# Performance work log

Measured on AMD Instinct MI355X. Metric: run time of the kernel, lower is better.

The kernel has to match this reference:

```python
import jax, jax.numpy as jnp
import numpy as np

D = 128
BITS = 3
N_LEVELS = 1 << BITS  # 8
BATCH = 262144
EPS = 1e-8


def _rotation_matrix(skew_params):
    """Cayley map: A skew-symmetric from strict-upper-tri params, R = (I+A)^{-1}(I-A)."""
    iu = np.triu_indices(D, k=1)
    A = jnp.zeros((D, D), dtype=skew_params.dtype).at[iu].set(skew_params)
    A = A - A.T
    I = jnp.eye(D, dtype=skew_params.dtype)
    # torch.linalg.solve(I + A, I - A) -> R with (I + A) @ R = (I - A)
    return jnp.linalg.solve(I + A, I - A)


def setup_inputs() -> dict:
    key = jax.random.key(0)
    k1, k2, k3 = jax.random.split(key, 3)
    x = jax.random.normal(k1, (BATCH, D), dtype=jnp.float32)
    # small init so Cayley rotation stays well-conditioned (torch init is zeros)
    skew_params = jax.random.normal(k2, (D * (D - 1) // 2,), dtype=jnp.float32) * 0.05
    # Lloyd-Max centroids are a sorted 1-D codebook of 2^bits levels
    centroids = jnp.sort(jax.random.normal(k3, (N_LEVELS,), dtype=jnp.float32))
    running_mean = jnp.zeros((D,), dtype=jnp.float32)
    return {"x": x, "skew_params": skew_params, "centroids": centroids,
            "running_mean": running_mean}


def reference(x, skew_params, centroids, running_mean):
    R = _rotation_matrix(skew_params)                      # (D, D) orthogonal
    mean = jax.lax.stop_gradient(running_mean)             # buffer, detached in torch
    x_c = x - mean                                         # (B, D)
    norms = jnp.maximum(jnp.linalg.norm(x_c, axis=-1, keepdims=True), EPS)
    x_unit = x_c / norms
    x_rot = x_unit @ R.T                                   # rotate
    # STE quantize: argmin-distance gather == one_hot @ centroids
    idx = jnp.argmin(jnp.abs(x_rot[..., None] - centroids), axis=-1)  # (B, D)
    x_quant = x_rot - jax.lax.stop_gradient(x_rot) + jnp.take(centroids, idx)
    x_recon = (x_quant @ R) * norms + mean                 # unrotate, rescale, recenter
    return x_recon
```

## Files before the change

### kernel.cpp

```cpp
#include <hip/hip_runtime.h>

#define BATCH 262144
#define MARGIN 1e-5f
#define LIST_CAP (1u<<20)

typedef __attribute__((ext_vector_type(8))) short short8;
typedef __attribute__((ext_vector_type(16))) float f32x16;


__device__ __forceinline__ unsigned f2bf(float f) {
  unsigned u = __float_as_uint(f);
  return (u + 0x7FFFu + ((u >> 16) & 1u)) >> 16;
}

__global__ __attribute__((amdgpu_waves_per_eu(4, 4))) __launch_bounds__(1024)
void kpre32(const float* __restrict__ skew, double* __restrict__ M64,
            double* __restrict__ Y64, unsigned int* __restrict__ counter)
{
  __shared__ float colk[2][128];
  __shared__ float pivrow[128];
  const int tid = threadIdx.x;
  const int i = tid >> 3;
  const int s = tid & 7;
  if (tid == 0) *counter = 0;

  float M[16];
  #pragma unroll
  for (int e = 0; e < 16; ++e) {
    int j = s + 8*e;
    float v;
    if (i == j)      v = 1.0f;
    else if (i < j)  v =  skew[i*127 - (i*(i-1))/2 + (j - i - 1)];
    else             v = -skew[j*127 - (j*(j-1))/2 + (i - j - 1)];
    M[e] = v;
    M64[i*128 + j] = (double)v;
  }
  if (s == 0) colk[0][i] = M[0];
  __syncthreads();

  for (int k = 0; k < 128; ++k) {
    const int p = k & 1, np = p ^ 1;
    const int ns = (k + 1) & 7, ne = (k + 1) >> 3;
    if (i == k) {
      float rec = 1.0f / colk[p][k];
      #pragma unroll
      for (int e = 0; e < 16; ++e) {
        int j = s + 8*e;
        float v = (j == k) ? 1.0f : M[e];
        v *= rec;
        M[e] = v;
        pivrow[j] = v;
      }
      if (s == ns && k < 127) colk[np][i] = M[ne];
    }
    __syncthreads();
    if (i != k) {
      float f = colk[p][i];
      #pragma unroll
      for (int e = 0; e < 16; ++e) {
        int j = s + 8*e;
        float v = (j == k) ? 0.0f : M[e];
        M[e] = fmaf(-f, pivrow[j], v);
      }
      if (s == ns && k < 127) colk[np][i] = M[ne];
    }
    __syncthreads();
  }

  #pragma unroll
  for (int e = 0; e < 16; ++e) {
    int j = s + 8*e;
    Y64[i*128 + j] = (double)M[e];
  }
}

__global__ __launch_bounds__(256, 2)
void kref(const double* __restrict__ M64, const double* __restrict__ Yin,
          double* __restrict__ Yout, double* __restrict__ Rt64,
          unsigned short* __restrict__ img, const int final_pass)
{
  __shared__ double Yc[128][17];
  __shared__ double T[128][17];
  const int t = threadIdx.x;
  const int c0 = blockIdx.x * 16;

  #pragma unroll
  for (int u = 0; u < 8; ++u) {
    int idx = u*256 + t;
    int row = idx >> 4, cc = idx & 15;
    Yc[row][cc] = Yin[row*128 + c0 + cc];
  }
  __syncthreads();

  const int m = t >> 1;
  const int h = (t & 1) * 8;

  double a0=0,a1=0,a2=0,a3=0,a4=0,a5=0,a6=0,a7=0;
  for (int j = 0; j < 128; ++j) {
    double mv = M64[m*128 + j];
    a0 = fma(mv, Yc[j][h+0], a0);  a1 = fma(mv, Yc[j][h+1], a1);
    a2 = fma(mv, Yc[j][h+2], a2);  a3 = fma(mv, Yc[j][h+3], a3);
    a4 = fma(mv, Yc[j][h+4], a4);  a5 = fma(mv, Yc[j][h+5], a5);
    a6 = fma(mv, Yc[j][h+6], a6);  a7 = fma(mv, Yc[j][h+7], a7);
  }
  T[m][h+0]=a0; T[m][h+1]=a1; T[m][h+2]=a2; T[m][h+3]=a3;
  T[m][h+4]=a4; T[m][h+5]=a5; T[m][h+6]=a6; T[m][h+7]=a7;
  __syncthreads();

  double b0=0,b1=0,b2=0,b3=0,b4=0,b5=0,b6=0,b7=0;
  for (int j = 0; j < 128; ++j) {
    double yv = Yin[m*128 + j];
    b0 = fma(yv, T[j][h+0], b0);  b1 = fma(yv, T[j][h+1], b1);
    b2 = fma(yv, T[j][h+2], b2);  b3 = fma(yv, T[j][h+3], b3);
    b4 = fma(yv, T[j][h+4], b4);  b5 = fma(yv, T[j][h+5], b5);
    b6 = fma(yv, T[j][h+6], b6);  b7 = fma(yv, T[j][h+7], b7);
  }

  double y2[8] = { 2.0*Yc[m][h+0]-b0, 2.0*Yc[m][h+1]-b1, 2.0*Yc[m][h+2]-b2,
                   2.0*Yc[m][h+3]-b3, 2.0*Yc[m][h+4]-b4, 2.0*Yc[m][h+5]-b5,
                   2.0*Yc[m][h+6]-b6, 2.0*Yc[m][h+7]-b7 };

  if (!final_pass) {
    #pragma unroll
    for (int c = 0; c < 8; ++c) Yout[m*128 + c0 + h + c] = y2[c];
  } else {
    #pragma unroll
    for (int c = 0; c < 8; ++c) {
      const int i = m, j = c0 + h + c;
      double v = 2.0*y2[c] - ((i == j) ? 1.0 : 0.0);
      Rt64[j*128 + i] = v;
      float r32 = (float)v;
      unsigned hh = f2bf(r32);
      unsigned ll = f2bf(r32 - __uint_as_float(hh << 16));
      int off1 = (((i>>5)*8 + (j>>4))*64 + ((((j>>3)&1)<<5) | (i&31)))*8 + (j&7);
      img[off1]          = (unsigned short)hh;
      img[16384 + off1]  = (unsigned short)ll;
      int off2 = (((j>>5)*8 + (i>>4))*64 + ((((i>>3)&1)<<5) | (j&31)))*8 + (i&7);
      img[32768 + off2]  = (unsigned short)hh;
      img[49152 + off2]  = (unsigned short)ll;
    }
  }
}

#define MM3(ACC, XH, XL, BH, BL)                                        \
  ACC = __builtin_amdgcn_mfma_f32_32x32x16_bf16(XH, BH, ACC, 0, 0, 0);  \
  ACC = __builtin_amdgcn_mfma_f32_32x32x16_bf16(XL, BH, ACC, 0, 0, 0);  \
  ACC = __builtin_amdgcn_mfma_f32_32x32x16_bf16(XH, BL, ACC, 0, 0, 0);

#define LGKM_BAR()                                                      \
  asm volatile("s_waitcnt lgkmcnt(0)" ::: "memory");                    \
  __builtin_amdgcn_s_barrier();                                         \
  __builtin_amdgcn_sched_barrier(0);

__global__ __launch_bounds__(256, 2)
void kmain(const float* __restrict__ x, const float* __restrict__ mean,
           const float* __restrict__ cent, const unsigned short* __restrict__ img,
           float* __restrict__ out,
           unsigned int* __restrict__ counter, unsigned int* __restrict__ list)
{
  __shared__ __align__(16) unsigned short Xh[2][32*128];
  __shared__ __align__(16) unsigned short Xl[2][32*128];
  __shared__ __align__(16) unsigned short Qh[2][32*128];
  __shared__ __align__(16) unsigned short Ql[2][32*128];
  __shared__ float norms[4][32];
  __shared__ float invs[4][32];

  const int tid = threadIdx.x, lane = tid & 63, w = tid >> 6;
  const int al = lane & 31, ah = lane >> 5;

  short8 B1h[8], B1l[8], B2h[8], B2l[8];
  #pragma unroll
  for (int t = 0; t < 8; ++t) {
    size_t o = (size_t)((w*8 + t)*64 + lane)*8;
    B1h[t] = *(const short8*)(img +         o);
    B1l[t] = *(const short8*)(img + 16384 + o);
    B2h[t] = *(const short8*)(img + 32768 + o);
    B2l[t] = *(const short8*)(img + 49152 + o);
  }

  const float c0 = cent[0], c1 = cent[1], c2 = cent[2], c3 = cent[3];
  const float c4 = cent[4], c5 = cent[5], c6 = cent[6], c7 = cent[7];
  const float mid0 = 0.5f*(c0+c1), mid1 = 0.5f*(c1+c2), mid2 = 0.5f*(c2+c3),
              mid3 = 0.5f*(c3+c4), mid4 = 0.5f*(c4+c5), mid5 = 0.5f*(c5+c6),
              mid6 = 0.5f*(c6+c7);
  unsigned qt0, qt1, qt2, qt3, qt4, qt5, qt6, qt7;
  {
    #define PS(C, QT) { unsigned h = f2bf(C); float hf = __uint_as_float(h<<16); \
                        QT = (h<<16) | f2bf((C) - hf); }
    PS(c0,qt0) PS(c1,qt1) PS(c2,qt2) PS(c3,qt3)
    PS(c4,qt4) PS(c5,qt5) PS(c6,qt6) PS(c7,qt7)
    #undef PS
  }

  const float2 mean2 = *(const float2*)(mean + 2*lane);
  const float meanv = mean[w*32 + al];

  const int row0 = blockIdx.x * 256;

  float2 xpf[8];
  #pragma unroll
  for (int rr = 0; rr < 8; ++rr)
    xpf[rr] = *(const float2*)(x + (size_t)(row0 + w*8 + rr)*128 + 2*lane);

  const bool own = (((al >> 2) & 1) == ah);
  const int rrq = al - 4*ah;
  const int gsel = (rrq & 3) + 4*(rrq >> 3);

  for (int ch = 0; ch < 8; ++ch) {
    const int chb = row0 + ch*32;
    const int p = ch & 1;

    float2 xn[8];
    if (ch < 7) {
      #pragma unroll
      for (int rr = 0; rr < 8; ++rr)
        xn[rr] = *(const float2*)(x + (size_t)(chb + 32 + w*8 + rr)*128 + 2*lane);
    }
    #pragma unroll
    for (int rr = 0; rr < 8; ++rr) {
      const int r = w*8 + rr;
      float a = xpf[rr].x - mean2.x;
      float b = xpf[rr].y - mean2.y;
      unsigned ph, pl;
      asm("v_cvt_pk_bf16_f32 %0, %1, %2" : "=v"(ph) : "v"(a), "v"(b));
      float ha = __uint_as_float(ph << 16);
      float hb = __uint_as_float(ph & 0xFFFF0000u);
      float ra = a - ha, rb = b - hb;
      asm("v_cvt_pk_bf16_f32 %0, %1, %2" : "=v"(pl) : "v"(ra), "v"(rb));
      unsigned off = ((unsigned)(r*256 + 4*lane)) ^ (((unsigned)(r & 7)) << 4);
      *(unsigned*)((char*)&Xh[p][0] + off) = ph;
      *(unsigned*)((char*)&Xl[p][0] + off) = pl;
    }
    #pragma unroll
    for (int rr = 0; rr < 8; ++rr) xpf[rr] = xn[rr];
    LGKM_BAR();

    f32x16 accN, accA, accB;
    #pragma unroll
    for (int g = 0; g < 16; ++g) { accN[g] = 0.0f; accA[g] = 0.0f; accB[g] = 0.0f; }
    __builtin_amdgcn_s_setprio(1);
    #pragma unroll
    for (int t = 0; t < 8; ++t) {
      unsigned fb = ((unsigned)(al*256 + t*32 + ah*16)) ^ (((unsigned)(al & 7)) << 4);
      short8 xh = *(const short8*)((const char*)&Xh[p][0] + fb);
      short8 xl = *(const short8*)((const char*)&Xl[p][0] + fb);
      accN = __builtin_amdgcn_mfma_f32_32x32x16_bf16(xh, xh, accN, 0, 0, 0);
      accN = __builtin_amdgcn_mfma_f32_32x32x16_bf16(xl, xh, accN, 0, 0, 0);
      accN = __builtin_amdgcn_mfma_f32_32x32x16_bf16(xh, xl, accN, 0, 0, 0);
      if (t & 1) { MM3(accB, xh, xl, B1h[t], B1l[t]); }
      else       { MM3(accA, xh, xl, B1h[t], B1l[t]); }
    }
    __builtin_amdgcn_s_setprio(0);
    #pragma unroll
    for (int g = 0; g < 16; ++g) accA[g] += accB[g];

    {
      float s2 = accN[0];
      #pragma unroll
      for (int e = 1; e < 16; ++e) s2 = (gsel == e) ? accN[e] : s2;
      if (own) {
        float n = fmaxf(sqrtf(s2), 1e-8f);
        norms[w][al] = n;
        invs[w][al]  = 1.0f / n;
      }
    }
    asm volatile("s_waitcnt lgkmcnt(0)" ::: "memory");

    unsigned qp[16];
    unsigned flags = 0;
    #pragma unroll
    for (int g = 0; g < 16; ++g) {
      const int r = (g & 3) + 8*(g >> 2) + 4*ah;
      float xr = accA[g] * invs[w][r];
      unsigned q = qt0;
      q = (xr > mid0) ? qt1 : q;  q = (xr > mid1) ? qt2 : q;
      q = (xr > mid2) ? qt3 : q;  q = (xr > mid3) ? qt4 : q;
      q = (xr > mid4) ? qt5 : q;  q = (xr > mid5) ? qt6 : q;
      q = (xr > mid6) ? qt7 : q;
      float dm = fabsf(xr - mid0);
      dm = fminf(dm, fabsf(xr - mid1)); dm = fminf(dm, fabsf(xr - mid2));
      dm = fminf(dm, fabsf(xr - mid3)); dm = fminf(dm, fabsf(xr - mid4));
      dm = fminf(dm, fabsf(xr - mid5)); dm = fminf(dm, fabsf(xr - mid6));
      qp[g] = q;
      flags |= (dm < MARGIN) ? (1u << g) : 0u;
    }
    #pragma unroll
    for (int g = 0; g < 16; ++g) {
      const int rq = (g & 3) + 8*(g >> 2) + 4*ah;
      unsigned off = ((unsigned)(rq*256 + (w*32 + al)*2)) ^ (((unsigned)(rq & 7)) << 4);
      *(unsigned short*)((char*)&Qh[p][0] + off) = (unsigned short)(qp[g] >> 16);
      *(unsigned short*)((char*)&Ql[p][0] + off) = (unsigned short)(qp[g] & 0xFFFFu);
    }
    if (__builtin_amdgcn_ballot_w64(flags != 0)) {
      #pragma unroll
      for (int g = 0; g < 16; ++g) {
        unsigned long long b = __ballot((flags >> g) & 1u);
        if (b) {
          const int rq = (g & 3) + 8*(g >> 2) + 4*ah;
          unsigned base = 0;
          if (lane == 0) base = atomicAdd(counter, (unsigned)__popcll(b));
          base = (unsigned)__shfl((int)base, 0);
          if ((flags >> g) & 1u) {
            unsigned pp = base + (unsigned)__popcll(b & ((1ull << lane) - 1ull));
            if (pp < LIST_CAP) list[pp] = (unsigned)(chb + rq);
          }
        }
      }
    }
    LGKM_BAR();

    f32x16 acc2, acc3;
    #pragma unroll
    for (int g = 0; g < 16; ++g) { acc2[g] = 0.0f; acc3[g] = 0.0f; }
    __builtin_amdgcn_s_setprio(1);
    #pragma unroll
    for (int t = 0; t < 8; ++t) {
      unsigned fb = ((unsigned)(al*256 + t*32 + ah*16)) ^ (((unsigned)(al & 7)) << 4);
      short8 xh = *(const short8*)((const char*)&Qh[p][0] + fb);
      short8 xl = *(const short8*)((const char*)&Ql[p][0] + fb);
      if (t & 1) { MM3(acc3, xh, xl, B2h[t], B2l[t]); }
      else       { MM3(acc2, xh, xl, B2h[t], B2l[t]); }
    }
    __builtin_amdgcn_s_setprio(0);

    #pragma unroll
    for (int g = 0; g < 16; ++g) {
      const int rq = (g & 3) + 8*(g >> 2) + 4*ah;
      float o = fmaf(acc2[g] + acc3[g], norms[w][rq], meanv);
      out[(size_t)(chb + rq)*128 + w*32 + al] = o;
    }
  }
}

__global__ __launch_bounds__(256)
void kfix(const float* __restrict__ x, const float* __restrict__ mean,
          const float* __restrict__ cent, const double* __restrict__ Rt64,
          float* __restrict__ out,
          const unsigned int* __restrict__ counter,
          const unsigned int* __restrict__ list)
{
  __shared__ double xs[4][128];
  __shared__ double qs[4][128];
  const int tid = threadIdx.x, lane = tid & 63, w = tid >> 6;

  unsigned cnt = *counter;
  if (cnt > LIST_CAP) cnt = LIST_CAP;

  const double cc0 = (double)cent[0], cc1 = (double)cent[1], cc2 = (double)cent[2],
               cc3 = (double)cent[3], cc4 = (double)cent[4], cc5 = (double)cent[5],
               cc6 = (double)cent[6], cc7 = (double)cent[7];
  const double m0 = 0.5*(cc0+cc1), m1 = 0.5*(cc1+cc2), m2 = 0.5*(cc2+cc3),
               m3 = 0.5*(cc3+cc4), m4 = 0.5*(cc4+cc5), m5 = 0.5*(cc5+cc6),
               m6 = 0.5*(cc6+cc7);

  const unsigned gw = blockIdx.x*4 + w, stride = gridDim.x*4;
  for (unsigned e = gw; e < cnt; e += stride) {
    const int row = (int)list[e];
    const float* xr = x + (size_t)row*128;
    const int j0 = 2*lane;

    double a = (double)xr[j0]   - (double)mean[j0];
    double b = (double)xr[j0+1] - (double)mean[j0+1];
    double s = a*a + b*b;
    s += __shfl_xor(s, 1);  s += __shfl_xor(s, 2);  s += __shfl_xor(s, 4);
    s += __shfl_xor(s, 8);  s += __shfl_xor(s, 16); s += __shfl_xor(s, 32);
    double n = sqrt(s);
    if (n < 1e-8) n = 1e-8;
    double inv = 1.0 / n;
    xs[w][j0]   = a * inv;
    xs[w][j0+1] = b * inv;
    asm volatile("s_waitcnt lgkmcnt(0)" ::: "memory");

    double acc0 = 0.0, acc1 = 0.0;
    for (int j = 0; j < 128; ++j) {
      double xj = xs[w][j];
      acc0 = fma(xj, Rt64[j*128 + j0],     acc0);
      acc1 = fma(xj, Rt64[j*128 + j0 + 1], acc1);
    }
    double q0 = cc0;
    q0 = (acc0 > m0) ? cc1 : q0;  q0 = (acc0 > m1) ? cc2 : q0;
    q0 = (acc0 > m2) ? cc3 : q0;  q0 = (acc0 > m3) ? cc4 : q0;
    q0 = (acc0 > m4) ? cc5 : q0;  q0 = (acc0 > m5) ? cc6 : q0;
    q0 = (acc0 > m6) ? cc7 : q0;
    double q1 = cc0;
    q1 = (acc1 > m0) ? cc1 : q1;  q1 = (acc1 > m1) ? cc2 : q1;
    q1 = (acc1 > m2) ? cc3 : q1;  q1 = (acc1 > m3) ? cc4 : q1;
    q1 = (acc1 > m4) ? cc5 : q1;  q1 = (acc1 > m5) ? cc6 : q1;
    q1 = (acc1 > m6) ? cc7 : q1;
    qs[w][j0]   = q0;
    qs[w][j0+1] = q1;
    asm volatile("s_waitcnt lgkmcnt(0)" ::: "memory");

    double o0 = 0.0, o1 = 0.0;
    for (int k = 0; k < 128; ++k) {
      double qk = qs[w][k];
      o0 = fma(qk, Rt64[j0*128 + k],       o0);
      o1 = fma(qk, Rt64[(j0+1)*128 + k],   o1);
    }
    out[(size_t)row*128 + j0]   = (float)fma(o0, n, (double)mean[j0]);
    out[(size_t)row*128 + j0+1] = (float)fma(o1, n, (double)mean[j0+1]);
  }
}

extern "C" void kernel_launch(void* const* d_in, const int* in_sizes, int n_in,
                              void* d_out, int out_size, void* d_ws, size_t ws_size,
                              hipStream_t stream)
{
  (void)in_sizes; (void)n_in; (void)out_size; (void)ws_size;
  const float* x    = (const float*)d_in[0];
  const float* skew = (const float*)d_in[1];
  const float* cent = (const float*)d_in[2];
  const float* mean = (const float*)d_in[3];
  float* out = (float*)d_out;

  char* ws = (char*)d_ws;
  double*         Rt64 = (double*)(ws);
  unsigned short* img  = (unsigned short*)(ws + 131072);
  unsigned int*   cntr = (unsigned int*)(ws + 262144);
  unsigned int*   list = (unsigned int*)(ws + 262912);
  double*         M64  = (double*)(ws + 4457216);
  double*         Y64  = (double*)(ws + 4588288);
  double*         Yb   = (double*)(ws + 4719360);

  kpre32<<<dim3(1),    dim3(1024), 0, stream>>>(skew, M64, Y64, cntr);
  kref  <<<dim3(8),    dim3(256),  0, stream>>>(M64, Y64, Yb, Rt64, img, 0);
  kref  <<<dim3(8),    dim3(256),  0, stream>>>(M64, Yb, Y64, Rt64, img, 1);
  kmain <<<dim3(1024), dim3(256),  0, stream>>>(x, mean, cent, img, out, cntr, list);
  kfix  <<<dim3(256),  dim3(256),  0, stream>>>(x, mean, cent, Rt64, out, cntr, list);
}
```

Before: 272.7 us.

## Precompute row norms in extra pre-kernel blocks, drop norm MFMAs from main kernel

Adds 256 extra blocks to the preprocessing kernel that compute each row's centered L2 norm and its reciprocal with shuffle reductions, writing both to workspace. The main kernel loads these per chunk into shared memory instead of computing norms with three extra bf16-split MFMAs per k-step. This is meant to cut about a third of the main kernel's matrix work, and the norm blocks can run alongside the single-block Cayley solve. The cost is an extra full read of x plus a small global buffer for norms and inverses.

Result: faster. 248.4 us (-8.9%).

```diff
diff --git a/kernel.cpp b/kernel.cpp
--- a/kernel.cpp
+++ b/kernel.cpp
@@ -14,12 +14,36 @@
 }
 
 __global__ __attribute__((amdgpu_waves_per_eu(4, 4))) __launch_bounds__(1024)
-void kpre32(const float* __restrict__ skew, double* __restrict__ M64,
-            double* __restrict__ Y64, unsigned int* __restrict__ counter)
+void kpre(const float* __restrict__ skew, const float* __restrict__ x,
+          const float* __restrict__ mean, double* __restrict__ M64,
+          double* __restrict__ Y64, float* __restrict__ normg,
+          float* __restrict__ invg, unsigned int* __restrict__ counter)
 {
+  const int tid = threadIdx.x;
+
+  if (blockIdx.x != 0) {
+    const int b  = blockIdx.x - 1;
+    const int wv = tid >> 6, ln = tid & 63;
+    const int rowbase = b*1024 + wv*64;
+    const float2 mv = *(const float2*)(mean + 2*ln);
+    for (int i = 0; i < 64; ++i) {
+      const int row = rowbase + i;
+      float2 xv = *(const float2*)(x + (size_t)row*128 + 2*ln);
+      float a = xv.x - mv.x, c = xv.y - mv.y;
+      float sq = fmaf(a, a, c*c);
+      sq += __shfl_xor(sq, 1);  sq += __shfl_xor(sq, 2);  sq += __shfl_xor(sq, 4);
+      sq += __shfl_xor(sq, 8);  sq += __shfl_xor(sq, 16); sq += __shfl_xor(sq, 32);
+      if (ln == 0) {
+        float n = fmaxf(sqrtf(sq), 1e-8f);
+        normg[row] = n;
+        invg[row]  = 1.0f / n;
+      }
+    }
+    return;
+  }
+
   __shared__ float colk[2][128];
   __shared__ float pivrow[128];
-  const int tid = threadIdx.x;
   const int i = tid >> 3;
   const int s = tid & 7;
   if (tid == 0) *counter = 0;
@@ -155,6 +179,7 @@
 __global__ __launch_bounds__(256, 2)
 void kmain(const float* __restrict__ x, const float* __restrict__ mean,
            const float* __restrict__ cent, const unsigned short* __restrict__ img,
+           const float* __restrict__ normg, const float* __restrict__ invg,
            float* __restrict__ out,
            unsigned int* __restrict__ counter, unsigned int* __restrict__ list)
 {
@@ -202,14 +227,14 @@
   for (int rr = 0; rr < 8; ++rr)
     xpf[rr] = *(const float2*)(x + (size_t)(row0 + w*8 + rr)*128 + 2*lane);
 
-  const bool own = (((al >> 2) & 1) == ah);
-  const int rrq = al - 4*ah;
-  const int gsel = (rrq & 3) + 4*(rrq >> 3);
-
   for (int ch = 0; ch < 8; ++ch) {
     const int chb = row0 + ch*32;
     const int p = ch & 1;
 
+    if (ah == 0) {
+      norms[w][al] = normg[chb + al];
+      invs[w][al]  = invg[chb + al];
+    }
     float2 xn[8];
     if (ch < 7) {
       #pragma unroll
@@ -235,36 +260,21 @@
     for (int rr = 0; rr < 8; ++rr) xpf[rr] = xn[rr];
     LGKM_BAR();
 
-    f32x16 accN, accA, accB;
-    #pragma unroll
-    for (int g = 0; g < 16; ++g) { accN[g] = 0.0f; accA[g] = 0.0f; accB[g] = 0.0f; }
+    f32x16 accA, accB;
+    #pragma unroll
+    for (int g = 0; g < 16; ++g) { accA[g] = 0.0f; accB[g] = 0.0f; }
     __builtin_amdgcn_s_setprio(1);
     #pragma unroll
     for (int t = 0; t < 8; ++t) {
       unsigned fb = ((unsigned)(al*256 + t*32 + ah*16)) ^ (((unsigned)(al & 7)) << 4);
       short8 xh = *(const short8*)((const char*)&Xh[p][0] + fb);
       short8 xl = *(const short8*)((const char*)&Xl[p][0] + fb);
-      accN = __builtin_amdgcn_mfma_f32_32x32x16_bf16(xh, xh, accN, 0, 0, 0);
-      accN = __builtin_amdgcn_mfma_f32_32x32x16_bf16(xl, xh, accN, 0, 0, 0);
-      accN = __builtin_amdgcn_mfma_f32_32x32x16_bf16(xh, xl, accN, 0, 0, 0);
       if (t & 1) { MM3(accB, xh, xl, B1h[t], B1l[t]); }
       else       { MM3(accA, xh, xl, B1h[t], B1l[t]); }
     }
     __builtin_amdgcn_s_setprio(0);
     #pragma unroll
     for (int g = 0; g < 16; ++g) accA[g] += accB[g];
-
-    {
-      float s2 = accN[0];
-      #pragma unroll
-      for (int e = 1; e < 16; ++e) s2 = (gsel == e) ? accN[e] : s2;
-      if (own) {
-        float n = fmaxf(sqrtf(s2), 1e-8f);
-        norms[w][al] = n;
-        invs[w][al]  = 1.0f / n;
-      }
-    }
-    asm volatile("s_waitcnt lgkmcnt(0)" ::: "memory");
 
     unsigned qp[16];
     unsigned flags = 0;
@@ -414,17 +424,21 @@
   float* out = (float*)d_out;
 
   char* ws = (char*)d_ws;
-  double*         Rt64 = (double*)(ws);
-  unsigned short* img  = (unsigned short*)(ws + 131072);
-  unsigned int*   cntr = (unsigned int*)(ws + 262144);
-  unsigned int*   list = (unsigned int*)(ws + 262912);
-  double*         M64  = (double*)(ws + 4457216);
-  double*         Y64  = (double*)(ws + 4588288);
-  double*         Yb   = (double*)(ws + 4719360);
-
-  kpre32<<<dim3(1),    dim3(1024), 0, stream>>>(skew, M64, Y64, cntr);
-  kref  <<<dim3(8),    dim3(256),  0, stream>>>(M64, Y64, Yb, Rt64, img, 0);
-  kref  <<<dim3(8),    dim3(256),  0, stream>>>(M64, Yb, Y64, Rt64, img, 1);
-  kmain <<<dim3(1024), dim3(256),  0, stream>>>(x, mean, cent, img, out, cntr, list);
-  kfix  <<<dim3(256),  dim3(256),  0, stream>>>(x, mean, cent, Rt64, out, cntr, list);
-}
+  double*         Rt64  = (double*)(ws);
+  unsigned short* img   = (unsigned short*)(ws + 131072);
+  unsigned int*   cntr  = (unsigned int*)(ws + 262144);
+  unsigned int*   list  = (unsigned int*)(ws + 262912);
+  double*         M64   = (double*)(ws + 4457216);
+  double*         Y64   = (double*)(ws + 4588288);
+  double*         Yb    = (double*)(ws + 4719360);
+  float*          normg = (float*)(ws + 4850432);
+  float*          invg  = (float*)(ws + 5899008);
+
+  kpre <<<dim3(257),  dim3(1024), 0, stream>>>(skew, x, mean, M64, Y64,
+                                               normg, invg, cntr);
+  kref <<<dim3(8),    dim3(256),  0, stream>>>(M64, Y64, Yb, Rt64, img, 0);
+  kref <<<dim3(8),    dim3(256),  0, stream>>>(M64, Yb, Y64, Rt64, img, 1);
+  kmain<<<dim3(1024), dim3(256),  0, stream>>>(x, mean, cent, img, normg, invg,
+                                               out, cntr, list);
+  kfix <<<dim3(256),  dim3(256),  0, stream>>>(x, mean, cent, Rt64, out, cntr, list);
+}
```
